# Optimization experiments

Measured on AMD Instinct MI355X. Metric: run time of the kernel, lower is better.

## Reference

```python
import jax, jax.numpy as jnp
import numpy as np

N_NODES = 10000
N_EDGES = 320000
NFEAT, NHID, NCLASS = 512, 256, 40


def setup_inputs() -> dict:
    key = jax.random.key(0)
    ks = jax.random.split(key, 8)
    x = jax.random.normal(ks[0], (N_NODES, NFEAT), dtype=jnp.float32)
    edge_src = jax.random.randint(ks[1], (N_EDGES,), 0, N_NODES, dtype=jnp.int32)
    edge_dst = jax.random.randint(ks[2], (N_EDGES,), 0, N_NODES, dtype=jnp.int32)
    edge_w = jax.random.uniform(ks[3], (N_EDGES,), dtype=jnp.float32)
    W1 = jax.random.normal(ks[4], (NFEAT, NHID), dtype=jnp.float32) * (1.0 / np.sqrt(NFEAT))
    b1 = jax.random.normal(ks[5], (NHID,), dtype=jnp.float32) * 0.01
    W2 = jax.random.normal(ks[6], (NHID, NCLASS), dtype=jnp.float32) * (1.0 / np.sqrt(NHID))
    b2 = jax.random.normal(ks[7], (NCLASS,), dtype=jnp.float32) * 0.01
    return {"x": x, "edge_src": edge_src, "edge_dst": edge_dst, "edge_w": edge_w,
            "W1": W1, "b1": b1, "W2": W2, "b2": b2}


def _spmm(edge_src, edge_dst, edge_w, h):
    # out[i] = sum_{e: dst_e == i} w_e * h[src_e]   (sparse adj @ h)
    msgs = h[edge_src] * edge_w[:, None]            # [E, d]
    return jax.ops.segment_sum(msgs, edge_dst, num_segments=h.shape[0])


def reference(x, edge_src, edge_dst, edge_w, W1, b1, W2, b2):
    # Layer 1: GraphConvolution(nfeat->nhid) with ReLU (dropout = identity in eval)
    h = jax.nn.relu(_spmm(edge_src, edge_dst, edge_w, x @ W1) + b1)
    # Layer 2: GraphConvolution(nhid->nclass), identity activation
    out = _spmm(edge_src, edge_dst, edge_w, h @ W2) + b2
    return jax.nn.log_softmax(out, axis=1)
```

## Files before the change

kernel.cpp:

```cpp
#include <hip/hip_runtime.h>
#include <hip/hip_bf16.h>
#include <math.h>

#define N_NODES 10000
#define MPAD    10112
#define N_EDGES 320000
#define NFEAT   512
#define NHID    256
#define NCLASS  40
#define SLOT    96
#define CSTRIDE 16
#define NBM1    158
#define NG1     (NBM1 * 2)
#define EB      ((N_EDGES + 255) / 256)

typedef short  short8  __attribute__((ext_vector_type(8)));
typedef float  floatx4 __attribute__((ext_vector_type(4)));

__device__ __forceinline__ unsigned short f2b(float f) {
  __hip_bfloat16 h = __float2bfloat16(f);
  unsigned short u; __builtin_memcpy(&u, &h, 2); return u;
}
__device__ __forceinline__ float b2f(unsigned short u) {
  return __uint_as_float(((unsigned)u) << 16);
}
__device__ __forceinline__ short8 pack8(float4 a, float4 b) {
  short8 r;
  r[0] = (short)f2b(a.x); r[1] = (short)f2b(a.y); r[2] = (short)f2b(a.z); r[3] = (short)f2b(a.w);
  r[4] = (short)f2b(b.x); r[5] = (short)f2b(b.y); r[6] = (short)f2b(b.z); r[7] = (short)f2b(b.w);
  return r;
}


__global__ __launch_bounds__(256) void prep_k(const float* __restrict__ W1,
                                              const float* __restrict__ W2,
                                              unsigned short* __restrict__ w1t,
                                              unsigned short* __restrict__ w2t,
                                              int* __restrict__ cnt) {
  int tid = blockIdx.x * 256 + threadIdx.x;
  if (tid < N_NODES * CSTRIDE) cnt[tid] = 0;
  const int nw1 = NFEAT * NHID;
  if (tid < nw1) {
    int k = tid / NHID, n = tid % NHID;
    w1t[n * NFEAT + k] = f2b(W1[tid]);
  } else if (tid < nw1 + 64 * NHID) {
    int j = tid - nw1;
    int n = j >> 8;
    int k = j & 255;
    w2t[j] = (n < NCLASS) ? f2b(W2[k * NCLASS + n]) : (unsigned short)0;
  }
}


__global__ __launch_bounds__(256) void gemm1_scatter_k(
    const float* __restrict__ x, const unsigned short* __restrict__ w1t,
    unsigned short* __restrict__ xw1b,
    const int* __restrict__ src, const int* __restrict__ dst,
    const float* __restrict__ w, int* __restrict__ cnt, int2* __restrict__ epk) {
  if (blockIdx.x >= NG1) {
    int e = (blockIdx.x - NG1) * 256 + threadIdx.x;
    if (e < N_EDGES) {
      int d = dst[e];
      int p = atomicAdd(&cnt[d << 4], 1);
      int2 pk; pk.x = src[e]; pk.y = __float_as_int(w[e]);
      epk[d * SLOT + p] = pk;
    }
    return;
  }

  __shared__ short8 As[2][64 * 4];
  __shared__ short8 Bs[2][128 * 4];

  const int t  = threadIdx.x;
  const int l  = t & 63;
  const int wc = t >> 6;
  const int bm = (blockIdx.x % NBM1) * 64;
  const int bn = (blockIdx.x / NBM1) * 128;

  const int rowA = t >> 2, sA = t & 3;
  const int rowB = t >> 1, sB = (t & 1) * 2;

  const float4 z4 = make_float4(0.f, 0.f, 0.f, 0.f);
  const floatx4 zero = {0.f, 0.f, 0.f, 0.f};
  floatx4 acc[4][2];
#pragma unroll
  for (int mi = 0; mi < 4; mi++) { acc[mi][0] = zero; acc[mi][1] = zero; }

  const int q = l >> 4;
  const bool arok = (bm + rowA) < N_NODES;
  const float* xrow = &x[(size_t)(bm + rowA) * NFEAT + sA * 8];
  const unsigned short* brow = &w1t[(size_t)(bn + rowB) * NFEAT + sB * 8];

  {
    float4 a0 = z4, a1 = z4;
    if (arok) { a0 = *(const float4*)(xrow); a1 = *(const float4*)(xrow + 4); }
    short8 b0 = *(const short8*)(brow);
    short8 b1 = *(const short8*)(brow + 8);
    As[0][rowA * 4 + (sA ^ (rowA & 3))] = pack8(a0, a1);
    Bs[0][rowB * 4 + ((sB    ) ^ (rowB & 3))] = b0;
    Bs[0][rowB * 4 + ((sB + 1) ^ (rowB & 3))] = b1;
  }

  for (int s = 0; s < 16; s++) {
    __syncthreads();
    const int cur = s & 1;
    float4 na0 = z4, na1 = z4;
    short8 nb0, nb1;
    const bool more = (s < 15);
    if (more) {
      const int k1 = (s + 1) * 32;
      if (arok) { na0 = *(const float4*)(xrow + k1); na1 = *(const float4*)(xrow + k1 + 4); }
      nb0 = *(const short8*)(brow + k1);
      nb1 = *(const short8*)(brow + k1 + 8);
    }

    short8 af[4], bf[2];
#pragma unroll
    for (int mi = 0; mi < 4; mi++) {
      int ar = mi * 16 + (l & 15);
      af[mi] = As[cur][ar * 4 + (q ^ (ar & 3))];
    }
#pragma unroll
    for (int ni = 0; ni < 2; ni++) {
      int bc = wc * 32 + ni * 16 + (l & 15);
      bf[ni] = Bs[cur][bc * 4 + (q ^ (bc & 3))];
    }
#pragma unroll
    for (int mi = 0; mi < 4; mi++)
#pragma unroll
      for (int ni = 0; ni < 2; ni++)
        acc[mi][ni] = __builtin_amdgcn_mfma_f32_16x16x32_bf16(af[mi], bf[ni], acc[mi][ni], 0, 0, 0);

    if (more) {
      const int nxt = cur ^ 1;
      As[nxt][rowA * 4 + (sA ^ (rowA & 3))] = pack8(na0, na1);
      Bs[nxt][rowB * 4 + ((sB    ) ^ (rowB & 3))] = nb0;
      Bs[nxt][rowB * 4 + ((sB + 1) ^ (rowB & 3))] = nb1;
    }
  }

#pragma unroll
  for (int mi = 0; mi < 4; mi++)
#pragma unroll
    for (int ni = 0; ni < 2; ni++) {
      int row = bm + mi * 16 + (l >> 4) * 4;
      int col = bn + wc * 32 + ni * 16 + (l & 15);
#pragma unroll
      for (int r = 0; r < 4; r++)
        xw1b[(size_t)(row + r) * NHID + col] = f2b(acc[mi][ni][r]);
    }
}


__global__ __launch_bounds__(256) void spmm1_k(const int* __restrict__ cnt,
                                               const int2* __restrict__ epk,
                                               const unsigned short* __restrict__ xw1b,
                                               const float* __restrict__ b1,
                                               unsigned short* __restrict__ h) {
  int bid     = blockIdx.x;
  int xcd     = bid & 7;
  int slice   = xcd >> 2;
  int quarter = xcd & 3;
  int wave    = threadIdx.x >> 6;
  int lane    = threadIdx.x & 63;
  int node    = (bid >> 3) * 4 + wave + quarter * 2500;
  int hh      = lane >> 5;
  int f       = lane & 31;
  int fbase   = slice * 128 + f * 4;

  int e0 = node * SLOT;
  int n  = cnt[node << 4];
  float a0 = 0.f, a1 = 0.f, a2 = 0.f, a3 = 0.f;
  for (int base = 0; base < n; base += 64) {
    int c2 = n - base; if (c2 > 64) c2 = 64;
    int2 my = make_int2(0, 0);
    if (lane < c2) my = epk[e0 + base + lane];
    int j = 0;
    for (; j + 8 <= c2; j += 8) {
#pragma unroll
      for (int p = 0; p < 4; p++) {
        int   idx = j + 2 * p + hh;
        int   s   = __shfl(my.x, idx);
        float wj  = __int_as_float(__shfl(my.y, idx));
        uint2 v = *(const uint2*)&xw1b[(size_t)s * NHID + fbase];
        a0 = fmaf(wj, b2f((unsigned short)(v.x & 0xffff)), a0);
        a1 = fmaf(wj, b2f((unsigned short)(v.x >> 16)),    a1);
        a2 = fmaf(wj, b2f((unsigned short)(v.y & 0xffff)), a2);
        a3 = fmaf(wj, b2f((unsigned short)(v.y >> 16)),    a3);
      }
    }
    for (; j < c2; j++) {
      int   s  = __shfl(my.x, j);
      float wj = __int_as_float(__shfl(my.y, j));
      if (hh == 0) {
        uint2 v = *(const uint2*)&xw1b[(size_t)s * NHID + fbase];
        a0 = fmaf(wj, b2f((unsigned short)(v.x & 0xffff)), a0);
        a1 = fmaf(wj, b2f((unsigned short)(v.x >> 16)),    a1);
        a2 = fmaf(wj, b2f((unsigned short)(v.y & 0xffff)), a2);
        a3 = fmaf(wj, b2f((unsigned short)(v.y >> 16)),    a3);
      }
    }
  }
  a0 += __shfl_xor(a0, 32);
  a1 += __shfl_xor(a1, 32);
  a2 += __shfl_xor(a2, 32);
  a3 += __shfl_xor(a3, 32);
  if (hh == 0) {
    a0 = fmaxf(a0 + b1[fbase + 0], 0.f);
    a1 = fmaxf(a1 + b1[fbase + 1], 0.f);
    a2 = fmaxf(a2 + b1[fbase + 2], 0.f);
    a3 = fmaxf(a3 + b1[fbase + 3], 0.f);
    uint2 po;
    po.x = ((unsigned)f2b(a1) << 16) | f2b(a0);
    po.y = ((unsigned)f2b(a3) << 16) | f2b(a2);
    *(uint2*)&h[(size_t)node * NHID + fbase] = po;
  }
}


__global__ __launch_bounds__(256) void gemm2_k(const unsigned short* __restrict__ h,
                                               const unsigned short* __restrict__ w2t,
                                               float* __restrict__ hw2) {
  __shared__ short8 As[64 * 4];
  __shared__ short8 Bs[64 * 4];

  const int t  = threadIdx.x;
  const int bm = blockIdx.x * 64;
  const int l  = t & 63;
  const int wv = t >> 6;
  const int wr = wv >> 1, wc = wv & 1;
  const int srow = t >> 2, sslot = t & 3;

  const floatx4 zero = {0.f, 0.f, 0.f, 0.f};
  floatx4 acc[2][2];
  acc[0][0] = zero; acc[0][1] = zero; acc[1][0] = zero; acc[1][1] = zero;

  const int q = l >> 4;

  for (int k0 = 0; k0 < NHID; k0 += 32) {
    short8 av = *(const short8*)&h  [(size_t)(bm + srow) * NHID + k0 + sslot * 8];
    short8 bv = *(const short8*)&w2t[(size_t)srow * NHID + k0 + sslot * 8];
    __syncthreads();
    As[srow * 4 + (sslot ^ (srow & 3))] = av;
    Bs[srow * 4 + (sslot ^ (srow & 3))] = bv;
    __syncthreads();

    short8 af[2], bf2[2];
#pragma unroll
    for (int mi = 0; mi < 2; mi++) {
      int ar = wr * 32 + mi * 16 + (l & 15);
      af[mi] = As[ar * 4 + (q ^ (ar & 3))];
    }
#pragma unroll
    for (int ni = 0; ni < 2; ni++) {
      int bc = wc * 32 + ni * 16 + (l & 15);
      bf2[ni] = Bs[bc * 4 + (q ^ (bc & 3))];
    }
#pragma unroll
    for (int mi = 0; mi < 2; mi++)
#pragma unroll
      for (int ni = 0; ni < 2; ni++)
        acc[mi][ni] = __builtin_amdgcn_mfma_f32_16x16x32_bf16(af[mi], bf2[ni], acc[mi][ni], 0, 0, 0);
  }

#pragma unroll
  for (int mi = 0; mi < 2; mi++)
#pragma unroll
    for (int ni = 0; ni < 2; ni++) {
      int row = bm + wr * 32 + mi * 16 + (l >> 4) * 4;
      int col = wc * 32 + ni * 16 + (l & 15);
#pragma unroll
      for (int r = 0; r < 4; r++)
        hw2[(size_t)(row + r) * 64 + col] = acc[mi][ni][r];
    }
}


__global__ __launch_bounds__(256) void spmm2_k(const int* __restrict__ cnt,
                                               const int2* __restrict__ epk,
                                               const float* __restrict__ hw2,
                                               const float* __restrict__ b2,
                                               float* __restrict__ out) {
  int wave = threadIdx.x >> 6;
  int lane = threadIdx.x & 63;
  int i    = blockIdx.x * 4 + wave;
  int hh   = lane >> 5;
  int c    = lane & 31;
  bool act = (c * 2 < NCLASS);
  int e0 = i * SLOT;
  int n  = cnt[i << 4];
  float a0 = 0.f, a1 = 0.f;
  for (int base = 0; base < n; base += 64) {
    int c2 = n - base; if (c2 > 64) c2 = 64;
    int2 my = make_int2(0, 0);
    if (lane < c2) my = epk[e0 + base + lane];
    int j = 0;
    for (; j + 8 <= c2; j += 8) {
#pragma unroll
      for (int p = 0; p < 4; p++) {
        int   idx = j + 2 * p + hh;
        int   s   = __shfl(my.x, idx);
        float wj  = __int_as_float(__shfl(my.y, idx));
        float2 v = *(const float2*)&hw2[(size_t)s * 64 + c * 2];
        a0 = fmaf(wj, v.x, a0);
        a1 = fmaf(wj, v.y, a1);
      }
    }
    for (; j < c2; j++) {
      int   s  = __shfl(my.x, j);
      float wj = __int_as_float(__shfl(my.y, j));
      if (hh == 0) {
        float2 v = *(const float2*)&hw2[(size_t)s * 64 + c * 2];
        a0 = fmaf(wj, v.x, a0);
        a1 = fmaf(wj, v.y, a1);
      }
    }
  }
  a0 += __shfl_xor(a0, 32);
  a1 += __shfl_xor(a1, 32);
  if (act) { a0 += b2[c * 2]; a1 += b2[c * 2 + 1]; }
  float mv = act ? fmaxf(a0, a1) : -INFINITY;
#pragma unroll
  for (int o = 16; o > 0; o >>= 1) mv = fmaxf(mv, __shfl_xor(mv, o));
  float ex = act ? (expf(a0 - mv) + expf(a1 - mv)) : 0.f;
#pragma unroll
  for (int o = 16; o > 0; o >>= 1) ex += __shfl_xor(ex, o);
  float ls = logf(ex);
  if (act && hh == 0) {
    float2 o2; o2.x = a0 - mv - ls; o2.y = a1 - mv - ls;
    *(float2*)&out[(size_t)i * NCLASS + c * 2] = o2;
  }
}


static inline size_t align256(size_t v) { return (v + 255) & ~(size_t)255; }

extern "C" void kernel_launch(void* const* d_in, const int* in_sizes, int n_in,
                              void* d_out, int out_size, void* d_ws, size_t ws_size,
                              hipStream_t stream) {
  const float* x        = (const float*)d_in[0];
  const int*   edge_src = (const int*)  d_in[1];
  const int*   edge_dst = (const int*)  d_in[2];
  const float* edge_w   = (const float*)d_in[3];
  const float* W1       = (const float*)d_in[4];
  const float* b1       = (const float*)d_in[5];
  const float* W2       = (const float*)d_in[6];
  const float* b2       = (const float*)d_in[7];
  float* out = (float*)d_out;

  char* ws = (char*)d_ws;
  size_t off = 0;
  unsigned short* w1t  = (unsigned short*)(ws + off); off = align256(off + (size_t)NFEAT * NHID * 2);
  unsigned short* w2t  = (unsigned short*)(ws + off); off = align256(off + (size_t)64 * NHID * 2);
  unsigned short* xw1b = (unsigned short*)(ws + off); off = align256(off + (size_t)MPAD * NHID * 2);
  unsigned short* h    = (unsigned short*)(ws + off); off = align256(off + (size_t)MPAD * NHID * 2);
  float* hw2 = (float*)(ws + off); off = align256(off + (size_t)MPAD * 64 * 4);
  int*   cnt = (int*)  (ws + off); off = align256(off + (size_t)N_NODES * CSTRIDE * 4);
  int2*  epk = (int2*) (ws + off); off = align256(off + (size_t)N_NODES * SLOT * 8);

  const int PREP_ITEMS = N_NODES * CSTRIDE;
  prep_k<<<(PREP_ITEMS + 255) / 256, 256, 0, stream>>>(W1, W2, w1t, w2t, cnt);

  gemm1_scatter_k<<<NG1 + EB, 256, 0, stream>>>(x, w1t, xw1b,
                                                edge_src, edge_dst, edge_w, cnt, epk);

  spmm1_k<<<5000, 256, 0, stream>>>(cnt, epk, xw1b, b1, h);

  gemm2_k<<<157, 256, 0, stream>>>(h, w2t, hw2);

  spmm2_k<<<2500, 256, 0, stream>>>(cnt, epk, hw2, b2, out);
}
```

Baseline: 69.20 us.

## Widen GEMM1 tile to full hidden width and give SpMM1 one wave per node

GEMM1 now uses 512-thread blocks that each compute a 64x256 output tile covering the whole hidden dimension, so x rows are loaded and converted once instead of twice. Half the threads load A and half load B, and the LDS B buffer doubles. The scatter blocks also grow to 512 edges each. SpMM1 drops the XCD-aware feature slicing and half-wave edge split: each wave now handles one node across all 256 features, which removes the cross-half reduction but may lose L2 locality across XCDs.

```diff
diff --git a/kernel.cpp b/kernel.cpp
--- a/kernel.cpp
+++ b/kernel.cpp
@@ -11,8 +11,7 @@
 #define SLOT    96
 #define CSTRIDE 16
 #define NBM1    158
-#define NG1     (NBM1 * 2)
-#define EB      ((N_EDGES + 255) / 256)
+#define EB2     ((N_EDGES + 511) / 512)
 
 typedef short  short8  __attribute__((ext_vector_type(8)));
 typedef float  floatx4 __attribute__((ext_vector_type(4)));
@@ -52,13 +51,13 @@
 }
 
 
-__global__ __launch_bounds__(256) void gemm1_scatter_k(
+__global__ __launch_bounds__(512) void gemm1_scatter_k(
     const float* __restrict__ x, const unsigned short* __restrict__ w1t,
     unsigned short* __restrict__ xw1b,
     const int* __restrict__ src, const int* __restrict__ dst,
     const float* __restrict__ w, int* __restrict__ cnt, int2* __restrict__ epk) {
-  if (blockIdx.x >= NG1) {
-    int e = (blockIdx.x - NG1) * 256 + threadIdx.x;
+  if (blockIdx.x >= NBM1) {
+    int e = (blockIdx.x - NBM1) * 512 + threadIdx.x;
     if (e < N_EDGES) {
       int d = dst[e];
       int p = atomicAdd(&cnt[d << 4], 1);
@@ -69,16 +68,16 @@
   }
 
   __shared__ short8 As[2][64 * 4];
-  __shared__ short8 Bs[2][128 * 4];
+  __shared__ short8 Bs[2][256 * 4];
 
   const int t  = threadIdx.x;
   const int l  = t & 63;
   const int wc = t >> 6;
-  const int bm = (blockIdx.x % NBM1) * 64;
-  const int bn = (blockIdx.x / NBM1) * 128;
-
-  const int rowA = t >> 2, sA = t & 3;
-  const int rowB = t >> 1, sB = (t & 1) * 2;
+  const int bm = blockIdx.x * 64;
+
+  const bool  isA  = (t < 256);
+  const int   rowA = t >> 2, sA = t & 3;
+  const int   rowB = t - 256;
 
   const float4 z4 = make_float4(0.f, 0.f, 0.f, 0.f);
   const floatx4 zero = {0.f, 0.f, 0.f, 0.f};
@@ -87,31 +86,34 @@
   for (int mi = 0; mi < 4; mi++) { acc[mi][0] = zero; acc[mi][1] = zero; }
 
   const int q = l >> 4;
-  const bool arok = (bm + rowA) < N_NODES;
+  const bool arok = isA && ((bm + rowA) < N_NODES);
   const float* xrow = &x[(size_t)(bm + rowA) * NFEAT + sA * 8];
-  const unsigned short* brow = &w1t[(size_t)(bn + rowB) * NFEAT + sB * 8];
-
-  {
+  const unsigned short* brow = &w1t[(size_t)rowB * NFEAT];
+
+  if (isA) {
     float4 a0 = z4, a1 = z4;
     if (arok) { a0 = *(const float4*)(xrow); a1 = *(const float4*)(xrow + 4); }
-    short8 b0 = *(const short8*)(brow);
-    short8 b1 = *(const short8*)(brow + 8);
     As[0][rowA * 4 + (sA ^ (rowA & 3))] = pack8(a0, a1);
-    Bs[0][rowB * 4 + ((sB    ) ^ (rowB & 3))] = b0;
-    Bs[0][rowB * 4 + ((sB + 1) ^ (rowB & 3))] = b1;
+  } else {
+#pragma unroll
+    for (int s = 0; s < 4; s++)
+      Bs[0][rowB * 4 + (s ^ (rowB & 3))] = *(const short8*)(brow + s * 8);
   }
 
   for (int s = 0; s < 16; s++) {
     __syncthreads();
     const int cur = s & 1;
     float4 na0 = z4, na1 = z4;
-    short8 nb0, nb1;
+    short8 nb[4];
     const bool more = (s < 15);
     if (more) {
       const int k1 = (s + 1) * 32;
-      if (arok) { na0 = *(const float4*)(xrow + k1); na1 = *(const float4*)(xrow + k1 + 4); }
-      nb0 = *(const short8*)(brow + k1);
-      nb1 = *(const short8*)(brow + k1 + 8);
+      if (isA) {
+        if (arok) { na0 = *(const float4*)(xrow + k1); na1 = *(const float4*)(xrow + k1 + 4); }
+      } else {
+#pragma unroll
+        for (int ss = 0; ss < 4; ss++) nb[ss] = *(const short8*)(brow + k1 + ss * 8);
+      }
     }
 
     short8 af[4], bf[2];
@@ -133,9 +135,13 @@
 
     if (more) {
       const int nxt = cur ^ 1;
-      As[nxt][rowA * 4 + (sA ^ (rowA & 3))] = pack8(na0, na1);
-      Bs[nxt][rowB * 4 + ((sB    ) ^ (rowB & 3))] = nb0;
-      Bs[nxt][rowB * 4 + ((sB + 1) ^ (rowB & 3))] = nb1;
+      if (isA) {
+        As[nxt][rowA * 4 + (sA ^ (rowA & 3))] = pack8(na0, na1);
+      } else {
+#pragma unroll
+        for (int ss = 0; ss < 4; ss++)
+          Bs[nxt][rowB * 4 + (ss ^ (rowB & 3))] = nb[ss];
+      }
     }
   }
 
@@ -144,7 +150,7 @@
 #pragma unroll
     for (int ni = 0; ni < 2; ni++) {
       int row = bm + mi * 16 + (l >> 4) * 4;
-      int col = bn + wc * 32 + ni * 16 + (l & 15);
+      int col = wc * 32 + ni * 16 + (l & 15);
 #pragma unroll
       for (int r = 0; r < 4; r++)
         xw1b[(size_t)(row + r) * NHID + col] = f2b(acc[mi][ni][r]);
@@ -157,16 +163,10 @@
                                                const unsigned short* __restrict__ xw1b,
                                                const float* __restrict__ b1,
                                                unsigned short* __restrict__ h) {
-  int bid     = blockIdx.x;
-  int xcd     = bid & 7;
-  int slice   = xcd >> 2;
-  int quarter = xcd & 3;
-  int wave    = threadIdx.x >> 6;
-  int lane    = threadIdx.x & 63;
-  int node    = (bid >> 3) * 4 + wave + quarter * 2500;
-  int hh      = lane >> 5;
-  int f       = lane & 31;
-  int fbase   = slice * 128 + f * 4;
+  int wave = threadIdx.x >> 6;
+  int lane = threadIdx.x & 63;
+  int node = blockIdx.x * 4 + wave;
+  int f0   = lane * 4;
 
   int e0 = node * SLOT;
   int n  = cnt[node << 4];
@@ -178,11 +178,10 @@
     int j = 0;
     for (; j + 8 <= c2; j += 8) {
 #pragma unroll
-      for (int p = 0; p < 4; p++) {
-        int   idx = j + 2 * p + hh;
-        int   s   = __shfl(my.x, idx);
-        float wj  = __int_as_float(__shfl(my.y, idx));
-        uint2 v = *(const uint2*)&xw1b[(size_t)s * NHID + fbase];
+      for (int p = 0; p < 8; p++) {
+        int   s  = __shfl(my.x, j + p);
+        float wj = __int_as_float(__shfl(my.y, j + p));
+        uint2 v = *(const uint2*)&xw1b[(size_t)s * NHID + f0];
         a0 = fmaf(wj, b2f((unsigned short)(v.x & 0xffff)), a0);
         a1 = fmaf(wj, b2f((unsigned short)(v.x >> 16)),    a1);
         a2 = fmaf(wj, b2f((unsigned short)(v.y & 0xffff)), a2);
@@ -192,29 +191,22 @@
     for (; j < c2; j++) {
       int   s  = __shfl(my.x, j);
       float wj = __int_as_float(__shfl(my.y, j));
-      if (hh == 0) {
-        uint2 v = *(const uint2*)&xw1b[(size_t)s * NHID + fbase];
-        a0 = fmaf(wj, b2f((unsigned short)(v.x & 0xffff)), a0);
-        a1 = fmaf(wj, b2f((unsigned short)(v.x >> 16)),    a1);
-        a2 = fmaf(wj, b2f((unsigned short)(v.y & 0xffff)), a2);
-        a3 = fmaf(wj, b2f((unsigned short)(v.y >> 16)),    a3);
-      }
-    }
-  }
-  a0 += __shfl_xor(a0, 32);
-  a1 += __shfl_xor(a1, 32);
-  a2 += __shfl_xor(a2, 32);
-  a3 += __shfl_xor(a3, 32);
-  if (hh == 0) {
-    a0 = fmaxf(a0 + b1[fbase + 0], 0.f);
-    a1 = fmaxf(a1 + b1[fbase + 1], 0.f);
-    a2 = fmaxf(a2 + b1[fbase + 2], 0.f);
-    a3 = fmaxf(a3 + b1[fbase + 3], 0.f);
-    uint2 po;
-    po.x = ((unsigned)f2b(a1) << 16) | f2b(a0);
-    po.y = ((unsigned)f2b(a3) << 16) | f2b(a2);
-    *(uint2*)&h[(size_t)node * NHID + fbase] = po;
-  }
+      uint2 v = *(const uint2*)&xw1b[(size_t)s * NHID + f0];
+      a0 = fmaf(wj, b2f((unsigned short)(v.x & 0xffff)), a0);
+      a1 = fmaf(wj, b2f((unsigned short)(v.x >> 16)),    a1);
+      a2 = fmaf(wj, b2f((unsigned short)(v.y & 0xffff)), a2);
+      a3 = fmaf(wj, b2f((unsigned short)(v.y >> 16)),    a3);
+    }
+  }
+  float4 bb = *(const float4*)&b1[f0];
+  a0 = fmaxf(a0 + bb.x, 0.f);
+  a1 = fmaxf(a1 + bb.y, 0.f);
+  a2 = fmaxf(a2 + bb.z, 0.f);
+  a3 = fmaxf(a3 + bb.w, 0.f);
+  uint2 po;
+  po.x = ((unsigned)f2b(a1) << 16) | f2b(a0);
+  po.y = ((unsigned)f2b(a3) << 16) | f2b(a2);
+  *(uint2*)&h[(size_t)node * NHID + f0] = po;
 }
 
 
@@ -361,10 +353,10 @@
   const int PREP_ITEMS = N_NODES * CSTRIDE;
   prep_k<<<(PREP_ITEMS + 255) / 256, 256, 0, stream>>>(W1, W2, w1t, w2t, cnt);
 
-  gemm1_scatter_k<<<NG1 + EB, 256, 0, stream>>>(x, w1t, xw1b,
-                                                edge_src, edge_dst, edge_w, cnt, epk);
-
-  spmm1_k<<<5000, 256, 0, stream>>>(cnt, epk, xw1b, b1, h);
+  gemm1_scatter_k<<<NBM1 + EB2, 512, 0, stream>>>(x, w1t, xw1b,
+                                                  edge_src, edge_dst, edge_w, cnt, epk);
+
+  spmm1_k<<<2500, 256, 0, stream>>>(cnt, epk, xw1b, b1, h);
 
   gemm2_k<<<157, 256, 0, stream>>>(h, w2t, hw2);
 
```

New measurement: 69.33 us. Within noise of the previous version (+0.2%).
